# Performance work log

Hardware: AMD Instinct MI355X
Metric: run time of the kernel (lower is better)

Reference implementation:

```python
import jax, jax.numpy as jnp
import numpy as np

E = 1024
H = 16
DH = E // H
FF = 4 * E
EPS = 1e-5


def _layer_norm(x, g, b):
    mu = jnp.mean(x, axis=-1, keepdims=True)
    var = jnp.var(x, axis=-1, keepdims=True)
    return (x - mu) * jax.lax.rsqrt(var + EPS) * g + b


def setup_inputs() -> dict:
    key = jax.random.key(0)
    ks = jax.random.split(key, 12)
    B, S = 2, 2048
    s_e = 1.0 / np.sqrt(E)
    s_f = 1.0 / np.sqrt(FF)
    return {
        "hidden_states": jax.random.normal(ks[0], (B, S, E), jnp.float32),
        "attention_mask": jnp.zeros((B, S), jnp.float32),
        "position_bias": jax.random.normal(ks[1], (H, S, S), jnp.float32) * 0.1,
        "Wq": jax.random.normal(ks[2], (E, E), jnp.float32) * s_e,
        "bq": jnp.zeros((E,), jnp.float32),
        "Wk": jax.random.normal(ks[3], (E, E), jnp.float32) * s_e,
        "bk": jnp.zeros((E,), jnp.float32),
        "Wv": jax.random.normal(ks[4], (E, E), jnp.float32) * s_e,
        "bv": jnp.zeros((E,), jnp.float32),
        "Wo": jax.random.normal(ks[5], (E, E), jnp.float32) * s_e,
        "bo": jnp.zeros((E,), jnp.float32),
        "ln1_g": jnp.ones((E,), jnp.float32),
        "ln1_b": jnp.zeros((E,), jnp.float32),
        "W1": jax.random.normal(ks[6], (E, FF), jnp.float32) * s_e,
        "b1": jnp.zeros((FF,), jnp.float32),
        "W2": jax.random.normal(ks[7], (FF, E), jnp.float32) * s_f,
        "b2": jnp.zeros((E,), jnp.float32),
        "ln2_g": jnp.ones((E,), jnp.float32),
        "ln2_b": jnp.zeros((E,), jnp.float32),
    }


def reference(hidden_states, attention_mask, position_bias, Wq, bq, Wk, bk, Wv, bv,
              Wo, bo, ln1_g, ln1_b, W1, b1, W2, b2, ln2_g, ln2_b):
    B, S, _ = hidden_states.shape
    x = hidden_states
    # QKV projections, split heads: [B, S, H, DH]
    q = (x @ Wq + bq).reshape(B, S, H, DH)
    k = (x @ Wk + bk).reshape(B, S, H, DH)
    v = (x @ Wv + bv).reshape(B, S, H, DH)
    # scores: [B, H, S, S]
    scores = jnp.einsum("bshd,bthd->bhst", q, k) / np.sqrt(DH).astype(np.float32)
    scores = scores + position_bias[None] + attention_mask[:, None, None, :]
    probs = jax.nn.softmax(scores, axis=-1)  # dropout is identity in eval
    ctx = jnp.einsum("bhst,bthd->bshd", probs, v).reshape(B, S, E)
    attn_out = ctx @ Wo + bo
    h = _layer_norm(x + attn_out, ln1_g, ln1_b)
    ffn = jax.nn.gelu(h @ W1 + b1, approximate=False) @ W2 + b2
    return _layer_norm(h + ffn, ln2_g, ln2_b)
```

## Files before the change

kernel.cpp:

```cpp
#include <hip/hip_runtime.h>
#include <stdint.h>

#define EDIM   1024
#define NHEAD  16
#define DHEAD  64
#define FFDIM  4096
#define SEQLEN 2048
#define NBATCH 2
#define MROWS  (NBATCH * SEQLEN)
#define NT     (SEQLEN / 64)

typedef __attribute__((ext_vector_type(8))) short bf16x8;
typedef __attribute__((ext_vector_type(4))) float f32x4;

static __device__ __forceinline__ unsigned short f2bf(float f) {
    union { float f; uint32_t u; } v; v.f = f;
    return (unsigned short)((v.u + 0x7fffu + ((v.u >> 16) & 1u)) >> 16);
}

static __device__ __forceinline__ void gload16(const void* g, void* s) {
    __builtin_amdgcn_global_load_lds(
        (const __attribute__((address_space(1))) unsigned int*)g,
        (__attribute__((address_space(3))) unsigned int*)s,
        16, 0, 0);
}

__global__ void k_cast_bf16(const float* __restrict__ in, unsigned short* __restrict__ out, int n4) {
    int i = blockIdx.x * blockDim.x + threadIdx.x;
    if (i < n4) {
        float4 v = ((const float4*)in)[i];
        ushort4 o;
        o.x = f2bf(v.x); o.y = f2bf(v.y); o.z = f2bf(v.z); o.w = f2bf(v.w);
        ((ushort4*)out)[i] = o;
    }
}

__global__ void k_transpose_cast(const float* __restrict__ in, unsigned short* __restrict__ out,
                                 int R, int C) {
    __shared__ float tile[32][33];
    int c0 = blockIdx.x * 32, r0 = blockIdx.y * 32;
    int tx = threadIdx.x, ty = threadIdx.y;
    #pragma unroll
    for (int i = 0; i < 32; i += 8)
        tile[ty + i][tx] = in[(size_t)(r0 + ty + i) * C + c0 + tx];
    __syncthreads();
    #pragma unroll
    for (int i = 0; i < 32; i += 8)
        out[(size_t)(c0 + ty + i) * R + r0 + tx] = f2bf(tile[tx][ty + i]);
}

__global__ void k_transpose_v(const unsigned short* __restrict__ V, int vstride,
                              unsigned short* __restrict__ Vt) {
    __shared__ unsigned short tile[32][33];
    const int bh = blockIdx.z, b = bh >> 4, h = bh & 15;
    const int s0 = blockIdx.x * 32, d0 = blockIdx.y * 32;
    const int tx = threadIdx.x, ty = threadIdx.y;
    #pragma unroll
    for (int i = 0; i < 32; i += 8)
        tile[ty + i][tx] = V[(size_t)(b * SEQLEN + s0 + ty + i) * vstride + h * DHEAD + d0 + tx];
    __syncthreads();
    #pragma unroll
    for (int i = 0; i < 32; i += 8)
        Vt[((size_t)(b * NHEAD + h) * DHEAD + d0 + ty + i) * SEQLEN + s0 + tx] = tile[tx][ty + i];
}

__global__ void k_concat_bias(const float* __restrict__ bq, const float* __restrict__ bk,
                              const float* __restrict__ bv, float* __restrict__ out) {
    int i = blockIdx.x * 256 + threadIdx.x;
    const float* src = (i < 1024) ? bq : (i < 2048) ? bk : bv;
    out[i] = src[i & 1023];
}

template <int TBM, int TBN, int EPI>
__global__ __launch_bounds__(256, 2) void k_gemm(
    const unsigned short* __restrict__ A,
    const unsigned short* __restrict__ Bt,
    const float* __restrict__ bias,
    void* __restrict__ Cout, int M, int N, int K)
{
    constexpr int MR = TBM / 32, NR = TBN / 32;
    __shared__ __attribute__((aligned(16))) unsigned short Asm[TBM * 64];
    __shared__ __attribute__((aligned(16))) unsigned short Bsm[TBN * 64];

    const int nbx = gridDim.x;
    const int flat = blockIdx.y * nbx + blockIdx.x;
    const int cpx = (nbx * gridDim.y) >> 3;
    const int swz = (flat & 7) * cpx + (flat >> 3);
    const int bx = swz % nbx, by = swz / nbx;

    const int row0 = by * TBM, col0 = bx * TBN;
    const int t = threadIdx.x;
    const int lane = t & 63, w = t >> 6;
    const int wm = w >> 1, wn = w & 1;
    const int l15 = lane & 15, l4 = lane >> 4;
    const int sr = lane >> 3, sc = (lane & 7) * 8;

    f32x4 acc[MR][NR];
    #pragma unroll
    for (int m = 0; m < MR; ++m)
        #pragma unroll
        for (int n = 0; n < NR; ++n) acc[m][n] = (f32x4){0.f, 0.f, 0.f, 0.f};

    for (int k0 = 0; k0 < K; k0 += 64) {
        #pragma unroll
        for (int i = 0; i < TBM / 32; ++i) {
            const int r = w * (TBM / 4) + i * 8;
            gload16(A + (size_t)(row0 + r + sr) * K + k0 + sc, &Asm[r * 64]);
        }
        #pragma unroll
        for (int i = 0; i < TBN / 32; ++i) {
            const int r = w * (TBN / 4) + i * 8;
            gload16(Bt + (size_t)(col0 + r + sr) * K + k0 + sc, &Bsm[r * 64]);
        }
        __syncthreads();
        #pragma unroll
        for (int kk = 0; kk < 64; kk += 32) {
            bf16x8 af[MR], bf[NR];
            #pragma unroll
            for (int m = 0; m < MR; ++m)
                af[m] = *(const bf16x8*)&Asm[(wm * (TBM / 2) + m * 16 + l15) * 64 + kk + l4 * 8];
            #pragma unroll
            for (int n = 0; n < NR; ++n)
                bf[n] = *(const bf16x8*)&Bsm[(wn * (TBN / 2) + n * 16 + l15) * 64 + kk + l4 * 8];
            #pragma unroll
            for (int m = 0; m < MR; ++m)
                #pragma unroll
                for (int n = 0; n < NR; ++n)
                    acc[m][n] = __builtin_amdgcn_mfma_f32_16x16x32_bf16(af[m], bf[n], acc[m][n], 0, 0, 0);
        }
        __syncthreads();
    }

    #pragma unroll
    for (int m = 0; m < MR; ++m) {
        int rb = row0 + wm * (TBM / 2) + m * 16 + l4 * 4;
        #pragma unroll
        for (int n = 0; n < NR; ++n) {
            int c = col0 + wn * (TBN / 2) + n * 16 + l15;
            float bv = bias[c];
            #pragma unroll
            for (int i = 0; i < 4; ++i) {
                float v = acc[m][n][i] + bv;
                if (EPI == 1) v = 0.5f * v * (1.0f + erff(v * 0.70710678118654752f));
                if (EPI == 2) ((float*)Cout)[(size_t)(rb + i) * N + c] = v;
                else          ((unsigned short*)Cout)[(size_t)(rb + i) * N + c] = f2bf(v);
            }
        }
    }
}

__global__ __launch_bounds__(512, 2) void k_attn(
    const unsigned short* __restrict__ QKV,
    const unsigned short* __restrict__ Vt,
    const float* __restrict__ pbias,
    const float* __restrict__ mask,
    unsigned short* __restrict__ Ctx)
{
    __shared__ __attribute__((aligned(16))) unsigned short Ksm[2][2][64 * 64];
    __shared__ __attribute__((aligned(16))) unsigned short Vsm[2][2][64 * 64];
    __shared__ __attribute__((aligned(16))) unsigned short Psm[8][16 * 32];

    const int flat = blockIdx.x;
    const int swz = (flat & 7) * 64 + (flat >> 3);
    const int qt = swz & 31;
    const int h  = swz >> 5;

    const int t = threadIdx.x;
    const int lane = t & 63, w = t >> 6;
    const int wb = w & 1;
    const int wq = (w >> 1) * 16;
    const int l15 = lane & 15, l4 = lane >> 4;
    const int qrow = qt * 64 + wq;

    const float* pbrow = pbias + ((size_t)h * SEQLEN + qrow + l4 * 4) * SEQLEN;
    const float* mrow  = mask + wb * SEQLEN;

    bf16x8 qf0, qf1;
    {
        const unsigned short* qp = QKV + (size_t)(wb * SEQLEN + qrow + l15) * (3 * EDIM) + h * DHEAD + l4 * 8;
        bf16x8 r0 = *(const bf16x8*)qp;
        bf16x8 r1 = *(const bf16x8*)(qp + 32);
        #pragma unroll
        for (int e = 0; e < 8; ++e) {
            union { uint32_t u; float f; } c0, c1;
            c0.u = (uint32_t)(unsigned short)r0[e] << 16;
            c1.u = (uint32_t)(unsigned short)r1[e] << 16;
            r0[e] = (short)f2bf(c0.f * 0.125f);
            r1[e] = (short)f2bf(c1.f * 0.125f);
        }
        qf0 = r0; qf1 = r1;
    }

    f32x4 oacc[4];
    #pragma unroll
    for (int nd = 0; nd < 4; ++nd) oacc[nd] = (f32x4){0.f, 0.f, 0.f, 0.f};
    float m_run[4] = {-1e30f, -1e30f, -1e30f, -1e30f};
    float l_run[4] = {0.f, 0.f, 0.f, 0.f};

    const int srow = lane >> 3;
    const int schk = lane & 7;
    const int r7 = l15 & 7;

    auto stage = [&](int buf, int kt) {
        const int kbase = kt * 64;
        #pragma unroll
        for (int j = 0; j < 4; ++j) {
            const int q  = w * 4 + j;
            const int kv = q >> 4;
            const int bb = (q >> 3) & 1;
            const int g  = q & 7;
            const int row = g * 8 + srow;
            const int cg  = (schk ^ (row & 7)) * 8;
            if (kv == 0)
                gload16(QKV + (size_t)(bb * SEQLEN + kbase + row) * (3 * EDIM) + EDIM + h * DHEAD + cg,
                        &Ksm[buf][bb][g * 512]);
            else
                gload16(Vt + ((size_t)((bb * NHEAD + h) * DHEAD) + row) * SEQLEN + kbase + cg,
                        &Vsm[buf][bb][g * 512]);
        }
    };

    auto compute = [&](int buf, int kt) {
        const int kbase = kt * 64;
        float p[4][4];
        float tmax[4] = {-1e30f, -1e30f, -1e30f, -1e30f};
        #pragma unroll
        for (int n = 0; n < 4; ++n) {
            const int scol = kbase + n * 16 + l15;
            const float mk = mrow[scol];
            f32x4 z;
            #pragma unroll
            for (int i = 0; i < 4; ++i) z[i] = pbrow[(size_t)i * SEQLEN + scol] + mk;
            bf16x8 kb0 = *(const bf16x8*)&Ksm[buf][wb][(n * 16 + l15) * 64 + ((l4 ^ r7) << 3)];
            bf16x8 kb1 = *(const bf16x8*)&Ksm[buf][wb][(n * 16 + l15) * 64 + (((4 + l4) ^ r7) << 3)];
            z = __builtin_amdgcn_mfma_f32_16x16x32_bf16(qf0, kb0, z, 0, 0, 0);
            z = __builtin_amdgcn_mfma_f32_16x16x32_bf16(qf1, kb1, z, 0, 0, 0);
            #pragma unroll
            for (int i = 0; i < 4; ++i) {
                p[n][i] = z[i];
                tmax[i] = fmaxf(tmax[i], z[i]);
            }
        }
        #pragma unroll
        for (int i = 0; i < 4; ++i) {
            float mv = tmax[i];
            #pragma unroll
            for (int off = 1; off < 16; off <<= 1) mv = fmaxf(mv, __shfl_xor(mv, off, 64));
            float mnew = fmaxf(m_run[i], mv);
            float alpha = __expf(m_run[i] - mnew);
            m_run[i] = mnew;
            float sum = 0.f;
            #pragma unroll
            for (int n = 0; n < 4; ++n) { p[n][i] = __expf(p[n][i] - mnew); sum += p[n][i]; }
            #pragma unroll
            for (int off = 1; off < 16; off <<= 1) sum += __shfl_xor(sum, off, 64);
            l_run[i] = l_run[i] * alpha + sum;
            #pragma unroll
            for (int nd = 0; nd < 4; ++nd) oacc[nd][i] *= alpha;
        }
        #pragma unroll
        for (int hh = 0; hh < 2; ++hh) {
            #pragma unroll
            for (int n = 0; n < 2; ++n)
                #pragma unroll
                for (int i = 0; i < 4; ++i) {
                    const int row = l4 * 4 + i;
                    const int cl = n * 16 + l15;
                    Psm[w][row * 32 + (((cl >> 3) ^ (row & 3)) << 3) + (cl & 7)] =
                        f2bf(p[2 * hh + n][i]);
                }
            bf16x8 pa = *(const bf16x8*)&Psm[w][l15 * 32 + ((l4 ^ (l15 & 3)) << 3)];
            #pragma unroll
            for (int nd = 0; nd < 4; ++nd) {
                bf16x8 vf = *(const bf16x8*)&Vsm[buf][wb][(nd * 16 + l15) * 64 + (((hh * 4 + l4) ^ r7) << 3)];
                oacc[nd] = __builtin_amdgcn_mfma_f32_16x16x32_bf16(pa, vf, oacc[nd], 0, 0, 0);
            }
        }
    };

    stage(0, 0);
    __syncthreads();
    int buf = 0;
    for (int kt = 0; kt < NT; ++kt) {
        stage(buf ^ 1, (kt + 1) & (NT - 1));
        compute(buf, kt);
        __syncthreads();
        buf ^= 1;
    }

    #pragma unroll
    for (int nd = 0; nd < 4; ++nd)
        #pragma unroll
        for (int i = 0; i < 4; ++i) {
            float v = oacc[nd][i] / l_run[i];
            Ctx[(size_t)(wb * SEQLEN + qrow + l4 * 4 + i) * EDIM + h * DHEAD + nd * 16 + l15] = f2bf(v);
        }
}

template <int WRITE_BF>
__global__ __launch_bounds__(256) void k_ln(
    const float* __restrict__ X, const float* __restrict__ T,
    const float* __restrict__ gam, const float* __restrict__ bet,
    float* __restrict__ Of, unsigned short* __restrict__ Ob)
{
    const int r = blockIdx.x;
    const int t = threadIdx.x;
    const size_t base = (size_t)r * EDIM + t * 4;
    float4 xv = *(const float4*)(X + base);
    float4 tv = *(const float4*)(T + base);
    float4 s = make_float4(xv.x + tv.x, xv.y + tv.y, xv.z + tv.z, xv.w + tv.w);
    float sum = s.x + s.y + s.z + s.w;
    float sq  = s.x * s.x + s.y * s.y + s.z * s.z + s.w * s.w;
    #pragma unroll
    for (int off = 1; off < 64; off <<= 1) {
        sum += __shfl_xor(sum, off, 64);
        sq  += __shfl_xor(sq,  off, 64);
    }
    __shared__ float red[8];
    const int lane = t & 63, w = t >> 6;
    if (lane == 0) { red[w] = sum; red[4 + w] = sq; }
    __syncthreads();
    sum = red[0] + red[1] + red[2] + red[3];
    sq  = red[4] + red[5] + red[6] + red[7];
    const float mu = sum * (1.0f / EDIM);
    const float var = sq * (1.0f / EDIM) - mu * mu;
    const float rs = rsqrtf(var + 1e-5f);
    float4 gv = *(const float4*)(gam + t * 4);
    float4 bv = *(const float4*)(bet + t * 4);
    float4 o = make_float4((s.x - mu) * rs * gv.x + bv.x,
                           (s.y - mu) * rs * gv.y + bv.y,
                           (s.z - mu) * rs * gv.z + bv.z,
                           (s.w - mu) * rs * gv.w + bv.w);
    *(float4*)(Of + base) = o;
    if (WRITE_BF) {
        ushort4 ob;
        ob.x = f2bf(o.x); ob.y = f2bf(o.y); ob.z = f2bf(o.z); ob.w = f2bf(o.w);
        *(ushort4*)(Ob + base) = ob;
    }
}

extern "C" void kernel_launch(void* const* d_in, const int* in_sizes, int n_in,
                              void* d_out, int out_size, void* d_ws, size_t ws_size,
                              hipStream_t stream) {
    const float* x    = (const float*)d_in[0];
    const float* mask = (const float*)d_in[1];
    const float* pb   = (const float*)d_in[2];
    const float* Wq = (const float*)d_in[3];  const float* bq = (const float*)d_in[4];
    const float* Wk = (const float*)d_in[5];  const float* bk = (const float*)d_in[6];
    const float* Wv = (const float*)d_in[7];  const float* bv = (const float*)d_in[8];
    const float* Wo = (const float*)d_in[9];  const float* bo = (const float*)d_in[10];
    const float* g1 = (const float*)d_in[11]; const float* be1 = (const float*)d_in[12];
    const float* W1 = (const float*)d_in[13]; const float* b1 = (const float*)d_in[14];
    const float* W2 = (const float*)d_in[15]; const float* b2 = (const float*)d_in[16];
    const float* g2 = (const float*)d_in[17]; const float* be2 = (const float*)d_in[18];
    float* out = (float*)d_out;

    char* ws = (char*)d_ws;
    const size_t MB = 1024 * 1024;
    unsigned short* qkv  = (unsigned short*)(ws + 0);
    unsigned short* gbf  = (unsigned short*)(ws + 0);
    unsigned short* xb   = (unsigned short*)(ws + 24 * MB);
    unsigned short* vt   = (unsigned short*)(ws + 24 * MB);
    unsigned short* wqt  = (unsigned short*)(ws + 32 * MB);
    unsigned short* wkt  = (unsigned short*)(ws + 34 * MB);
    unsigned short* wvt  = (unsigned short*)(ws + 36 * MB);
    unsigned short* wot  = (unsigned short*)(ws + 38 * MB);
    unsigned short* w1t  = (unsigned short*)(ws + 40 * MB);
    unsigned short* w2t  = (unsigned short*)(ws + 48 * MB);
    float*          bcat = (float*)(ws + 56 * MB);
    unsigned short* ctxb = (unsigned short*)(ws + 56 * MB);
    float*          t1   = (float*)(ws + 64 * MB);
    float*          hf   = (float*)(ws + 80 * MB);
    unsigned short* hb   = (unsigned short*)(ws + 96 * MB);

    const dim3 b256(256);
    const dim3 tb(32, 8);

    k_cast_bf16<<<dim3(MROWS * EDIM / 4 / 256), b256, 0, stream>>>(x, xb, MROWS * EDIM / 4);
    k_transpose_cast<<<dim3(EDIM / 32, EDIM / 32), tb, 0, stream>>>(Wq, wqt, EDIM, EDIM);
    k_transpose_cast<<<dim3(EDIM / 32, EDIM / 32), tb, 0, stream>>>(Wk, wkt, EDIM, EDIM);
    k_transpose_cast<<<dim3(EDIM / 32, EDIM / 32), tb, 0, stream>>>(Wv, wvt, EDIM, EDIM);
    k_transpose_cast<<<dim3(EDIM / 32, EDIM / 32), tb, 0, stream>>>(Wo, wot, EDIM, EDIM);
    k_transpose_cast<<<dim3(FFDIM / 32, EDIM / 32), tb, 0, stream>>>(W1, w1t, EDIM, FFDIM);
    k_transpose_cast<<<dim3(EDIM / 32, FFDIM / 32), tb, 0, stream>>>(W2, w2t, FFDIM, EDIM);
    k_concat_bias<<<dim3(12), b256, 0, stream>>>(bq, bk, bv, bcat);

    k_gemm<128, 128, 0><<<dim3(3 * EDIM / 128, MROWS / 128), b256, 0, stream>>>(
        xb, wqt, bcat, qkv, MROWS, 3 * EDIM, EDIM);
    k_transpose_v<<<dim3(SEQLEN / 32, DHEAD / 32, NBATCH * NHEAD), tb, 0, stream>>>(
        qkv + 2 * EDIM, 3 * EDIM, vt);

    k_attn<<<dim3(512), dim3(512), 0, stream>>>(qkv, vt, pb, mask, ctxb);

    k_gemm<128, 64, 2><<<dim3(EDIM / 64, MROWS / 128), b256, 0, stream>>>(
        ctxb, wot, bo, t1, MROWS, EDIM, EDIM);
    k_ln<1><<<dim3(MROWS), b256, 0, stream>>>(x, t1, g1, be1, hf, hb);
    k_gemm<128, 128, 1><<<dim3(FFDIM / 128, MROWS / 128), b256, 0, stream>>>(
        hb, w1t, b1, gbf, MROWS, FFDIM, EDIM);
    k_gemm<128, 64, 2><<<dim3(EDIM / 64, MROWS / 128), b256, 0, stream>>>(
        gbf, w2t, b2, t1, MROWS, EDIM, FFDIM);
    k_ln<0><<<dim3(MROWS), b256, 0, stream>>>(hf, t1, g2, be2, out, nullptr);
    (void)in_sizes; (void)n_in; (void)out_size; (void)ws_size;
}
```

Measured before the change: 402.4 us.

## Split-K the Wo and W2 GEMMs with larger tiles, summing partials in layernorm

The output-projection and FFN-down GEMMs now use 128x128 tiles with a two-way K split on blockIdx.z. Each split writes its own fp32 partial buffer, and the bias is added only by the first split. The layernorm kernel takes a second partial and sums both into the residual, so no separate reduction kernel is needed. The aim is larger tiles with more operand reuse at the same block count, at the cost of extra partial-buffer writes and reads and a bigger workspace.

```diff
diff --git a/kernel.cpp b/kernel.cpp
--- a/kernel.cpp
+++ b/kernel.cpp
@@ -71,7 +71,7 @@
     out[i] = src[i & 1023];
 }
 
-template <int TBM, int TBN, int EPI>
+template <int TBM, int TBN, int EPI, int SPLITK>
 __global__ __launch_bounds__(256, 2) void k_gemm(
     const unsigned short* __restrict__ A,
     const unsigned short* __restrict__ Bt,
@@ -87,6 +87,8 @@
     const int cpx = (nbx * gridDim.y) >> 3;
     const int swz = (flat & 7) * cpx + (flat >> 3);
     const int bx = swz % nbx, by = swz / nbx;
+    const int kz = (SPLITK > 1) ? blockIdx.z : 0;
+    const int Ksub = K / SPLITK;
 
     const int row0 = by * TBM, col0 = bx * TBN;
     const int t = threadIdx.x;
@@ -101,7 +103,7 @@
         #pragma unroll
         for (int n = 0; n < NR; ++n) acc[m][n] = (f32x4){0.f, 0.f, 0.f, 0.f};
 
-    for (int k0 = 0; k0 < K; k0 += 64) {
+    for (int k0 = kz * Ksub; k0 < (kz + 1) * Ksub; k0 += 64) {
         #pragma unroll
         for (int i = 0; i < TBM / 32; ++i) {
             const int r = w * (TBM / 4) + i * 8;
@@ -137,13 +139,17 @@
         #pragma unroll
         for (int n = 0; n < NR; ++n) {
             int c = col0 + wn * (TBN / 2) + n * 16 + l15;
-            float bv = bias[c];
+            float bv = (SPLITK == 1 || kz == 0) ? bias[c] : 0.0f;
             #pragma unroll
             for (int i = 0; i < 4; ++i) {
                 float v = acc[m][n][i] + bv;
                 if (EPI == 1) v = 0.5f * v * (1.0f + erff(v * 0.70710678118654752f));
-                if (EPI == 2) ((float*)Cout)[(size_t)(rb + i) * N + c] = v;
-                else          ((unsigned short*)Cout)[(size_t)(rb + i) * N + c] = f2bf(v);
+                if (EPI == 2) {
+                    float* outp = (float*)Cout + (size_t)kz * M * N;
+                    outp[(size_t)(rb + i) * N + c] = v;
+                } else {
+                    ((unsigned short*)Cout)[(size_t)(rb + i) * N + c] = f2bf(v);
+                }
             }
         }
     }
@@ -299,7 +305,7 @@
 
 template <int WRITE_BF>
 __global__ __launch_bounds__(256) void k_ln(
-    const float* __restrict__ X, const float* __restrict__ T,
+    const float* __restrict__ X, const float* __restrict__ T, const float* __restrict__ T2,
     const float* __restrict__ gam, const float* __restrict__ bet,
     float* __restrict__ Of, unsigned short* __restrict__ Ob)
 {
@@ -308,7 +314,9 @@
     const size_t base = (size_t)r * EDIM + t * 4;
     float4 xv = *(const float4*)(X + base);
     float4 tv = *(const float4*)(T + base);
-    float4 s = make_float4(xv.x + tv.x, xv.y + tv.y, xv.z + tv.z, xv.w + tv.w);
+    float4 t2 = *(const float4*)(T2 + base);
+    float4 s = make_float4(xv.x + tv.x + t2.x, xv.y + tv.y + t2.y,
+                           xv.z + tv.z + t2.z, xv.w + tv.w + t2.w);
     float sum = s.x + s.y + s.z + s.w;
     float sq  = s.x * s.x + s.y * s.y + s.z * s.z + s.w * s.w;
     #pragma unroll
@@ -359,8 +367,6 @@
     const size_t MB = 1024 * 1024;
     unsigned short* qkv  = (unsigned short*)(ws + 0);
     unsigned short* gbf  = (unsigned short*)(ws + 0);
-    unsigned short* xb   = (unsigned short*)(ws + 24 * MB);
-    unsigned short* vt   = (unsigned short*)(ws + 24 * MB);
     unsigned short* wqt  = (unsigned short*)(ws + 32 * MB);
     unsigned short* wkt  = (unsigned short*)(ws + 34 * MB);
     unsigned short* wvt  = (unsigned short*)(ws + 36 * MB);
@@ -369,9 +375,12 @@
     unsigned short* w2t  = (unsigned short*)(ws + 48 * MB);
     float*          bcat = (float*)(ws + 56 * MB);
     unsigned short* ctxb = (unsigned short*)(ws + 56 * MB);
-    float*          t1   = (float*)(ws + 64 * MB);
-    float*          hf   = (float*)(ws + 80 * MB);
-    unsigned short* hb   = (unsigned short*)(ws + 96 * MB);
+    unsigned short* xb   = (unsigned short*)(ws + 64 * MB);
+    unsigned short* vt   = (unsigned short*)(ws + 64 * MB);
+    float*          pt0  = (float*)(ws + 72 * MB);
+    float*          pt1  = (float*)(ws + 88 * MB);
+    float*          hf   = (float*)(ws + 104 * MB);
+    unsigned short* hb   = (unsigned short*)(ws + 120 * MB);
 
     const dim3 b256(256);
     const dim3 tb(32, 8);
@@ -385,20 +394,20 @@
     k_transpose_cast<<<dim3(EDIM / 32, FFDIM / 32), tb, 0, stream>>>(W2, w2t, FFDIM, EDIM);
     k_concat_bias<<<dim3(12), b256, 0, stream>>>(bq, bk, bv, bcat);
 
-    k_gemm<128, 128, 0><<<dim3(3 * EDIM / 128, MROWS / 128), b256, 0, stream>>>(
+    k_gemm<128, 128, 0, 1><<<dim3(3 * EDIM / 128, MROWS / 128), b256, 0, stream>>>(
         xb, wqt, bcat, qkv, MROWS, 3 * EDIM, EDIM);
     k_transpose_v<<<dim3(SEQLEN / 32, DHEAD / 32, NBATCH * NHEAD), tb, 0, stream>>>(
         qkv + 2 * EDIM, 3 * EDIM, vt);
 
     k_attn<<<dim3(512), dim3(512), 0, stream>>>(qkv, vt, pb, mask, ctxb);
 
-    k_gemm<128, 64, 2><<<dim3(EDIM / 64, MROWS / 128), b256, 0, stream>>>(
-        ctxb, wot, bo, t1, MROWS, EDIM, EDIM);
-    k_ln<1><<<dim3(MROWS), b256, 0, stream>>>(x, t1, g1, be1, hf, hb);
-    k_gemm<128, 128, 1><<<dim3(FFDIM / 128, MROWS / 128), b256, 0, stream>>>(
+    k_gemm<128, 128, 2, 2><<<dim3(EDIM / 128, MROWS / 128, 2), b256, 0, stream>>>(
+        ctxb, wot, bo, pt0, MROWS, EDIM, EDIM);
+    k_ln<1><<<dim3(MROWS), b256, 0, stream>>>(x, pt0, pt1, g1, be1, hf, hb);
+    k_gemm<128, 128, 1, 1><<<dim3(FFDIM / 128, MROWS / 128), b256, 0, stream>>>(
         hb, w1t, b1, gbf, MROWS, FFDIM, EDIM);
-    k_gemm<128, 64, 2><<<dim3(EDIM / 64, MROWS / 128), b256, 0, stream>>>(
-        gbf, w2t, b2, t1, MROWS, EDIM, FFDIM);
-    k_ln<0><<<dim3(MROWS), b256, 0, stream>>>(hf, t1, g2, be2, out, nullptr);
+    k_gemm<128, 128, 2, 2><<<dim3(EDIM / 128, MROWS / 128, 2), b256, 0, stream>>>(
+        gbf, w2t, b2, pt0, MROWS, EDIM, FFDIM);
+    k_ln<0><<<dim3(MROWS), b256, 0, stream>>>(hf, pt0, pt1, g2, be2, out, nullptr);
     (void)in_sizes; (void)n_in; (void)out_size; (void)ws_size;
 }
```

Result: faster. 368.7 us (-8.4%).
